# Optimization experiments

Hardware: AMD Instinct MI355X
Metric: run time of the kernel (lower is better)

Reference implementation:

```python
import jax, jax.numpy as jnp
import numpy as np

NUM_ITERATIONS = 3


def squash(s, axis):
    # ||s||^2/(1+||s||^2) * s/||s||, standard CapsNet squash along `axis`
    sq = jnp.sum(s * s, axis=axis, keepdims=True)
    return (sq / (1.0 + sq)) * s / jnp.sqrt(sq)


def setup_inputs() -> dict:
    key = jax.random.key(0)
    k1, k2 = jax.random.split(key)
    x = jax.random.normal(k1, (512, 1152, 8), dtype=jnp.float32)
    W = jax.random.normal(k2, (1152, 10, 16, 8), dtype=jnp.float32)
    return {"x": x, "W": W}


def reference(x, W):
    # x: [B, I=1152, J=8]; W: [I, O=10, D=16, J]
    # u_hat[b,i,o,d] = sum_j W[i,o,d,j] * x[b,i,j]
    u_hat = jnp.einsum('iodj,bij->biod', W, x)  # [B, 1152, 10, 16]
    I, O = W.shape[0], W.shape[1]
    b_ij = jnp.zeros((I, O), dtype=u_hat.dtype)
    v = None
    for _ in range(NUM_ITERATIONS):
        # legacy F.softmax default on 4D [1,1152,10,1] -> dim=1 (input-capsule axis)
        c = jax.nn.softmax(b_ij, axis=0)  # [1152, 10]
        s = jnp.einsum('io,biod->bod', c, u_hat)  # [B, 10, 16]
        v = squash(s, axis=-1)  # [B, 10, 16]
        # agreement <u_hat, v>, averaged over batch
        agree = jnp.einsum('biod,bod->bio', u_hat, v)  # [B, 1152, 10]
        b_ij = b_ij + jnp.mean(agree, axis=0)
    # original returns v_j.squeeze(1): shape [B, 10, 16, 1]
    return v[..., None]
```

## Files before the change

### kernel.cpp

```cpp
#include <hip/hip_runtime.h>

#define BB 512
#define II 1152
#define OO 10
#define DD 16
#define JJ 8
#define OD 160
#define KK (II*JJ)

#define BT 64
#define NBT (BB/BT)
#define IC 16
#define NS (II/IC)

__global__ __launch_bounds__(256) void k_transpose(const float* __restrict__ x,
                                                   float* __restrict__ xT) {
  __shared__ float tile[32][33];
  int kb = blockIdx.x;
  int bb = blockIdx.y;
  int tx = threadIdx.x & 31, ty = threadIdx.x >> 5;
  int k0 = kb * 32, b0 = bb * 32;
#pragma unroll
  for (int r = ty; r < 32; r += 8)
    tile[r][tx] = x[(size_t)(b0 + r) * KK + k0 + tx];
  __syncthreads();
#pragma unroll
  for (int r = ty; r < 32; r += 8)
    xT[(size_t)(k0 + r) * BB + b0 + tx] = tile[tx][r];
}

__global__ __launch_bounds__(256) void k_fill(float* __restrict__ c) {
  c[blockIdx.x * 256 + threadIdx.x] = 1.0f / 1152.0f;
}

__global__ __launch_bounds__(256) void k_bupd_softmax(float* __restrict__ b_ij,
                                                      const float* __restrict__ agreep,
                                                      float* __restrict__ c) {
  int o = blockIdx.x, t = threadIdx.x;
  __shared__ float buf[II];
  __shared__ float red[4];
  float mx = -1e30f;
  for (int i = t; i < II; i += 256) {
    float a = 0.f;
#pragma unroll
    for (int d = 0; d < 16; ++d) a += agreep[(size_t)(o * 16 + d) * II + i];
    float val = b_ij[i * OO + o] + a * (1.0f / (float)BB);
    b_ij[i * OO + o] = val;
    buf[i] = val;
    mx = fmaxf(mx, val);
  }
  for (int off = 32; off; off >>= 1) mx = fmaxf(mx, __shfl_down(mx, off));
  if ((t & 63) == 0) red[t >> 6] = mx;
  __syncthreads();
  mx = fmaxf(fmaxf(red[0], red[1]), fmaxf(red[2], red[3]));
  __syncthreads();
  float sum = 0.f;
  for (int i = t; i < II; i += 256) {
    float e = expf(buf[i] - mx);
    buf[i] = e;
    sum += e;
  }
  for (int off = 32; off; off >>= 1) sum += __shfl_down(sum, off);
  if ((t & 63) == 0) red[t >> 6] = sum;
  __syncthreads();
  sum = red[0] + red[1] + red[2] + red[3];
  float inv = 1.0f / sum;
  for (int i = t; i < II; i += 256) c[i * OO + o] = buf[i] * inv;
}

__global__ __launch_bounds__(256) void k_s_part(const float* __restrict__ xT,
                                                const float* __restrict__ W,
                                                const float* __restrict__ c,
                                                float* __restrict__ spart) {
  __shared__ float smem[64 * 164];
  int bt = blockIdx.x;
  int ch = blockIdx.y;
  int b0 = bt * BT;
  int i0 = ch * IC;
  int t = threadIdx.x;
  int bq = t & 15;
  int og = t >> 4;
  float acc[4][10];
#pragma unroll
  for (int bb = 0; bb < 4; ++bb)
#pragma unroll
    for (int r = 0; r < 10; ++r) acc[bb][r] = 0.f;

  for (int g = 0; g < 4; ++g) {
    int ig = i0 + g * 4;
    __syncthreads();
#pragma unroll
    for (int q = 0; q < 5; ++q) {
      int e4 = q * 256 + t;
      int ii = e4 / 320;
      int rem = e4 - ii * 320;
      int o = rem >> 5;
      float cv = c[(ig + ii) * OO + o];
      float4 w4 = *(const float4*)&W[(size_t)(ig + ii) * 1280 + rem * 4];
      float4 r4;
      r4.x = w4.x * cv; r4.y = w4.y * cv; r4.z = w4.z * cv; r4.w = w4.w * cv;
      *(float4*)&smem[ii * 1280 + rem * 4] = r4;
    }
    __syncthreads();
#pragma unroll
    for (int ii = 0; ii < 4; ++ii) {
      int i = ig + ii;
      float xr[8][4];
#pragma unroll
      for (int j = 0; j < 8; ++j) {
        float4 q4 = *(const float4*)&xT[(size_t)(i * 8 + j) * BB + b0 + bq * 4];
        xr[j][0] = q4.x; xr[j][1] = q4.y; xr[j][2] = q4.z; xr[j][3] = q4.w;
      }
      const float* wrow = &smem[ii * 1280 + og * 80];
#pragma unroll
      for (int r = 0; r < 10; ++r) {
        float4 w0 = *(const float4*)&wrow[r * 8];
        float4 w1 = *(const float4*)&wrow[r * 8 + 4];
#pragma unroll
        for (int bb = 0; bb < 4; ++bb) {
          float a = acc[bb][r];
          a = fmaf(xr[0][bb], w0.x, a);
          a = fmaf(xr[1][bb], w0.y, a);
          a = fmaf(xr[2][bb], w0.z, a);
          a = fmaf(xr[3][bb], w0.w, a);
          a = fmaf(xr[4][bb], w1.x, a);
          a = fmaf(xr[5][bb], w1.y, a);
          a = fmaf(xr[6][bb], w1.z, a);
          a = fmaf(xr[7][bb], w1.w, a);
          acc[bb][r] = a;
        }
      }
    }
  }
  __syncthreads();
#pragma unroll
  for (int bb = 0; bb < 4; ++bb)
#pragma unroll
    for (int r = 0; r < 10; ++r)
      smem[(bq * 4 + bb) * 164 + og * 10 + r] = acc[bb][r];
  __syncthreads();
  float* dst = &spart[(size_t)ch * BB * OD + (size_t)b0 * OD];
#pragma unroll
  for (int k2 = 0; k2 < 10; ++k2) {
    int idx = k2 * 256 + t;
    int row = idx / 40;
    int col4 = idx - row * 40;
    float4 val = *(const float4*)&smem[row * 164 + col4 * 4];
    *(float4*)&dst[row * 160 + col4 * 4] = val;
  }
}

__global__ __launch_bounds__(256) void k_squash(const float* __restrict__ spart,
                                                float* __restrict__ v) {
  int t = blockIdx.x * 256 + threadIdx.x;
  float s = 0.f;
#pragma unroll 8
  for (int ns = 0; ns < NS; ++ns) s += spart[(size_t)ns * (BB * OD) + t];
  float sq = s * s;
  sq += __shfl_xor(sq, 1);
  sq += __shfl_xor(sq, 2);
  sq += __shfl_xor(sq, 4);
  sq += __shfl_xor(sq, 8);
  float scale = sqrtf(sq) / (1.0f + sq);
  v[t] = s * scale;
}

__global__ __launch_bounds__(256) void k_G(const float* __restrict__ x,
                                           const float* __restrict__ v,
                                           float* __restrict__ Gp) {
  __shared__ float smem[32 * 160];
  int t = threadIdx.x;
  int bq = t & 7;
  int og = t >> 3;
  int k0 = blockIdx.x * 32;
  int bh = blockIdx.y;
  int bbase = bh * 256;

  float acc[4][5];
#pragma unroll
  for (int kk = 0; kk < 4; ++kk)
#pragma unroll
    for (int r = 0; r < 5; ++r) acc[kk][r] = 0.f;

  for (int ph = 0; ph < 8; ++ph) {
    int bc = bbase + ph * 32;
    __syncthreads();
#pragma unroll
    for (int p = 0; p < 5; ++p) {
      int idx = p * 256 + t;
      *(float4*)&smem[idx * 4] = *(const float4*)&v[(size_t)bc * 160 + idx * 4];
    }
    __syncthreads();
#pragma unroll 4
    for (int bi = 0; bi < 32; ++bi) {
      float4 x4 = *(const float4*)&x[(size_t)(bc + bi) * KK + k0 + bq * 4];
      const float* vrow = &smem[bi * 160 + og * 5];
      float xv[4] = {x4.x, x4.y, x4.z, x4.w};
#pragma unroll
      for (int r = 0; r < 5; ++r) {
        float vv_ = vrow[r];
#pragma unroll
        for (int kk = 0; kk < 4; ++kk)
          acc[kk][r] = fmaf(xv[kk], vv_, acc[kk][r]);
      }
    }
  }
#pragma unroll
  for (int r = 0; r < 5; ++r) {
    int od = og * 5 + r;
    float4 st = {acc[0][r], acc[1][r], acc[2][r], acc[3][r]};
    *(float4*)&Gp[((size_t)bh * OD + od) * KK + k0 + bq * 4] = st;
  }
}

__global__ __launch_bounds__(256) void k_WGred(const float* __restrict__ W,
                                               const float* __restrict__ Gp,
                                               float* __restrict__ agreep) {
  int od = blockIdx.x;
  int o = od >> 4, d = od & 15;
  int t = threadIdx.x;
  for (int ic = 0; ic < 5; ++ic) {
    int i = ic * 256 + t;
    if (i >= II) break;
    const float* gp0 = &Gp[(size_t)od * KK + (size_t)i * 8];
    const float* gp1 = gp0 + (size_t)OD * KK;
    float4 a0 = *(const float4*)gp0;
    float4 a1 = *(const float4*)(gp0 + 4);
    float4 b0 = *(const float4*)gp1;
    float4 b1 = *(const float4*)(gp1 + 4);
    float4 g0 = {a0.x + b0.x, a0.y + b0.y, a0.z + b0.z, a0.w + b0.w};
    float4 g1 = {a1.x + b1.x, a1.y + b1.y, a1.z + b1.z, a1.w + b1.w};
    const float* wp = &W[(size_t)((i * OO + o) * DD + d) * JJ];
    float4 w0 = *(const float4*)wp;
    float4 w1 = *(const float4*)(wp + 4);
    float acc = w0.x * g0.x + w0.y * g0.y + w0.z * g0.z + w0.w * g0.w +
                w1.x * g1.x + w1.y * g1.y + w1.z * g1.z + w1.w * g1.w;
    agreep[(size_t)od * II + i] = acc;
  }
}

extern "C" void kernel_launch(void* const* d_in, const int* in_sizes, int n_in,
                              void* d_out, int out_size, void* d_ws, size_t ws_size,
                              hipStream_t stream) {
  const float* x = (const float*)d_in[0];
  const float* W = (const float*)d_in[1];
  float* out = (float*)d_out;
  float* ws = (float*)d_ws;

  float* b_ij = ws;
  float* c    = ws + 11520;
  float* vv   = ws + 23040;
  float* xT   = ws + 186880;
  float* sp   = ws + 4905472;
  float* Gp   = sp;
  float* agreep = sp + 2949120;

  hipMemsetAsync(b_ij, 0, 11520 * sizeof(float), stream);
  k_transpose<<<dim3(288, 16), 256, 0, stream>>>(x, xT);
  k_fill<<<45, 256, 0, stream>>>(c);

  for (int it = 0; it < 3; ++it) {
    k_s_part<<<dim3(NBT, NS), 256, 0, stream>>>(xT, W, c, sp);
    k_squash<<<320, 256, 0, stream>>>(sp, it == 2 ? out : vv);
    if (it < 2) {
      k_G<<<dim3(288, 2), 256, 0, stream>>>(x, vv, Gp);
      k_WGred<<<160, 256, 0, stream>>>(W, Gp, agreep);
      k_bupd_softmax<<<OO, 256, 0, stream>>>(b_ij, agreep, c);
    }
  }
}
```

Before: 315.5 us.

## Prefetch W/c and v tiles into registers; split k_G over output halves

k_s_part now loads the next W and c chunk into registers while it computes on the current shared-memory tile, and shrinks its shared buffer by writing the result out in two halves. k_G is split across a new grid dimension for two output halves, using 128 threads and half the shared memory, and prefetches the next v slab into registers. The aim is to hide global load latency and raise occupancy, at the cost of more registers and k_G reading x twice.

```diff
diff --git a/kernel.cpp b/kernel.cpp
--- a/kernel.cpp
+++ b/kernel.cpp
@@ -72,7 +72,7 @@
                                                 const float* __restrict__ W,
                                                 const float* __restrict__ c,
                                                 float* __restrict__ spart) {
-  __shared__ float smem[64 * 164];
+  __shared__ float smem[5248];
   int bt = blockIdx.x;
   int ch = blockIdx.y;
   int b0 = bt * BT;
@@ -86,22 +86,41 @@
 #pragma unroll
     for (int r = 0; r < 10; ++r) acc[bb][r] = 0.f;
 
+  int s_ii[5], s_rem[5], s_o[5];
+#pragma unroll
+  for (int q = 0; q < 5; ++q) {
+    int e4 = q * 256 + t;
+    s_ii[q] = e4 / 320;
+    s_rem[q] = e4 - s_ii[q] * 320;
+    s_o[q] = s_rem[q] >> 5;
+  }
+  float4 wreg[5];
+  float creg[5];
+#pragma unroll
+  for (int q = 0; q < 5; ++q) {
+    wreg[q] = *(const float4*)&W[(size_t)(i0 + s_ii[q]) * 1280 + s_rem[q] * 4];
+    creg[q] = c[(i0 + s_ii[q]) * OO + s_o[q]];
+  }
+
   for (int g = 0; g < 4; ++g) {
     int ig = i0 + g * 4;
     __syncthreads();
 #pragma unroll
     for (int q = 0; q < 5; ++q) {
-      int e4 = q * 256 + t;
-      int ii = e4 / 320;
-      int rem = e4 - ii * 320;
-      int o = rem >> 5;
-      float cv = c[(ig + ii) * OO + o];
-      float4 w4 = *(const float4*)&W[(size_t)(ig + ii) * 1280 + rem * 4];
       float4 r4;
-      r4.x = w4.x * cv; r4.y = w4.y * cv; r4.z = w4.z * cv; r4.w = w4.w * cv;
-      *(float4*)&smem[ii * 1280 + rem * 4] = r4;
-    }
-    __syncthreads();
+      r4.x = wreg[q].x * creg[q]; r4.y = wreg[q].y * creg[q];
+      r4.z = wreg[q].z * creg[q]; r4.w = wreg[q].w * creg[q];
+      *(float4*)&smem[s_ii[q] * 1280 + s_rem[q] * 4] = r4;
+    }
+    __syncthreads();
+    if (g < 3) {
+      int ig2 = i0 + (g + 1) * 4;
+#pragma unroll
+      for (int q = 0; q < 5; ++q) {
+        wreg[q] = *(const float4*)&W[(size_t)(ig2 + s_ii[q]) * 1280 + s_rem[q] * 4];
+        creg[q] = c[(ig2 + s_ii[q]) * OO + s_o[q]];
+      }
+    }
 #pragma unroll
     for (int ii = 0; ii < 4; ++ii) {
       int i = ig + ii;
@@ -132,21 +151,26 @@
       }
     }
   }
-  __syncthreads();
-#pragma unroll
-  for (int bb = 0; bb < 4; ++bb)
-#pragma unroll
-    for (int r = 0; r < 10; ++r)
-      smem[(bq * 4 + bb) * 164 + og * 10 + r] = acc[bb][r];
-  __syncthreads();
-  float* dst = &spart[(size_t)ch * BB * OD + (size_t)b0 * OD];
-#pragma unroll
-  for (int k2 = 0; k2 < 10; ++k2) {
-    int idx = k2 * 256 + t;
-    int row = idx / 40;
-    int col4 = idx - row * 40;
-    float4 val = *(const float4*)&smem[row * 164 + col4 * 4];
-    *(float4*)&dst[row * 160 + col4 * 4] = val;
+#pragma unroll
+  for (int h = 0; h < 2; ++h) {
+    __syncthreads();
+    if ((bq >> 3) == h) {
+#pragma unroll
+      for (int bb = 0; bb < 4; ++bb)
+#pragma unroll
+        for (int r = 0; r < 10; ++r)
+          smem[((bq & 7) * 4 + bb) * 164 + og * 10 + r] = acc[bb][r];
+    }
+    __syncthreads();
+    float* dst = &spart[(size_t)ch * BB * OD + (size_t)(b0 + h * 32) * OD];
+#pragma unroll
+    for (int p = 0; p < 5; ++p) {
+      int idx = p * 256 + t;
+      int row = idx / 40;
+      int col4 = idx - row * 40;
+      float4 val = *(const float4*)&smem[row * 164 + col4 * 4];
+      *(float4*)&dst[row * 160 + col4 * 4] = val;
+    }
   }
 }
 
@@ -165,15 +189,17 @@
   v[t] = s * scale;
 }
 
-__global__ __launch_bounds__(256) void k_G(const float* __restrict__ x,
+__global__ __launch_bounds__(128) void k_G(const float* __restrict__ x,
                                            const float* __restrict__ v,
                                            float* __restrict__ Gp) {
-  __shared__ float smem[32 * 160];
+  __shared__ float smem[32 * 80];
   int t = threadIdx.x;
   int bq = t & 7;
   int og = t >> 3;
   int k0 = blockIdx.x * 32;
-  int bh = blockIdx.y;
+  int oh = blockIdx.y;
+  int bh = blockIdx.z;
+  int ob = oh * 80;
   int bbase = bh * 256;
 
   float acc[4][5];
@@ -181,20 +207,38 @@
   for (int kk = 0; kk < 4; ++kk)
 #pragma unroll
     for (int r = 0; r < 5; ++r) acc[kk][r] = 0.f;
+
+  float4 vreg[5];
+#pragma unroll
+  for (int p = 0; p < 5; ++p) {
+    int idx = p * 128 + t;
+    int b = idx / 20, col4 = idx - b * 20;
+    vreg[p] = *(const float4*)&v[(size_t)(bbase + b) * 160 + ob + col4 * 4];
+  }
 
   for (int ph = 0; ph < 8; ++ph) {
     int bc = bbase + ph * 32;
     __syncthreads();
 #pragma unroll
     for (int p = 0; p < 5; ++p) {
-      int idx = p * 256 + t;
-      *(float4*)&smem[idx * 4] = *(const float4*)&v[(size_t)bc * 160 + idx * 4];
-    }
-    __syncthreads();
+      int idx = p * 128 + t;
+      int b = idx / 20, col4 = idx - b * 20;
+      *(float4*)&smem[b * 80 + col4 * 4] = vreg[p];
+    }
+    __syncthreads();
+    if (ph < 7) {
+      int bc2 = bc + 32;
+#pragma unroll
+      for (int p = 0; p < 5; ++p) {
+        int idx = p * 128 + t;
+        int b = idx / 20, col4 = idx - b * 20;
+        vreg[p] = *(const float4*)&v[(size_t)(bc2 + b) * 160 + ob + col4 * 4];
+      }
+    }
 #pragma unroll 4
     for (int bi = 0; bi < 32; ++bi) {
       float4 x4 = *(const float4*)&x[(size_t)(bc + bi) * KK + k0 + bq * 4];
-      const float* vrow = &smem[bi * 160 + og * 5];
+      const float* vrow = &smem[bi * 80 + og * 5];
       float xv[4] = {x4.x, x4.y, x4.z, x4.w};
 #pragma unroll
       for (int r = 0; r < 5; ++r) {
@@ -207,7 +251,7 @@
   }
 #pragma unroll
   for (int r = 0; r < 5; ++r) {
-    int od = og * 5 + r;
+    int od = ob + og * 5 + r;
     float4 st = {acc[0][r], acc[1][r], acc[2][r], acc[3][r]};
     *(float4*)&Gp[((size_t)bh * OD + od) * KK + k0 + bq * 4] = st;
   }
@@ -263,7 +307,7 @@
     k_s_part<<<dim3(NBT, NS), 256, 0, stream>>>(xT, W, c, sp);
     k_squash<<<320, 256, 0, stream>>>(sp, it == 2 ? out : vv);
     if (it < 2) {
-      k_G<<<dim3(288, 2), 256, 0, stream>>>(x, vv, Gp);
+      k_G<<<dim3(288, 2, 2), 128, 0, stream>>>(x, vv, Gp);
       k_WGred<<<160, 256, 0, stream>>>(W, Gp, agreep);
       k_bupd_softmax<<<OO, 256, 0, stream>>>(b_ij, agreep, c);
     }
```

Result: slower. 350.9 us (+11.2%).
